# Optimization experiments

Hardware: AMD Instinct MI355X
Metric: run time of the kernel (lower is better)

## Reference

```python
import jax, jax.numpy as jnp
import numpy as np

N = 50000   # nodes
E = 600000  # edges (before self-loops)
D = 128     # input_dim
H = 128     # hidden_dim
NEG_SLOPE = 0.2  # GATConv default


def setup_inputs() -> dict:
    key = jax.random.key(0)
    ks = jax.random.split(key, 16)
    inp = {
        "x": jax.random.normal(ks[0], (N, D), jnp.float32),
        "edge_index": jax.random.randint(ks[1], (2, E), 0, N, dtype=jnp.int64),
        "edge_attr": jax.random.normal(ks[2], (E, 1), jnp.float32),
    }
    # GATConv params per layer: lin W [H,in] (no bias), att_src/att_dst [H],
    # lin_edge We [H,1] (no bias), att_edge [H], final bias b [H]
    def mk(k, shape, fan_in):
        return jax.random.normal(k, shape, jnp.float32) / np.sqrt(fan_in)
    ins = [D, H]
    ki = 3
    for i in range(2):
        cin = ins[i]
        inp[f"W{i}"] = mk(ks[ki], (H, cin), cin); ki += 1
        inp[f"att_src{i}"] = mk(ks[ki], (H,), H); ki += 1
        inp[f"att_dst{i}"] = mk(ks[ki], (H,), H); ki += 1
        inp[f"We{i}"] = mk(ks[ki], (H, 1), 1); ki += 1
        inp[f"att_e{i}"] = mk(ks[ki], (H,), H); ki += 1
        inp[f"b{i}"] = jnp.zeros((H,), jnp.float32)
    return inp


def _gat_forward(x, edge_index, edge_attr, params):
    # add self loops; self-loop edge_attr = mean of edge_attr (fill_value='mean')
    src = jnp.concatenate([edge_index[0], jnp.arange(N, dtype=edge_index.dtype)])
    dst = jnp.concatenate([edge_index[1], jnp.arange(N, dtype=edge_index.dtype)])
    ea = jnp.concatenate(
        [edge_attr, jnp.broadcast_to(edge_attr.mean(0, keepdims=True), (N, 1))], 0
    )  # [E+N, 1]

    def gat_layer(h, W, b, a_s, a_d, We, a_e):
        hp = h @ W.T                                   # [N, H]
        e_lin = ea @ We.T                              # [E+N, H]
        alpha = (hp @ a_s)[src] + (hp @ a_d)[dst] + e_lin @ a_e  # [E+N]
        alpha = jax.nn.leaky_relu(alpha, NEG_SLOPE)
        # segment softmax over destination nodes
        m = jax.ops.segment_max(alpha, dst, num_segments=N)
        m = jnp.where(jnp.isfinite(m), m, 0.0)
        w = jnp.exp(alpha - m[dst])
        denom = jax.ops.segment_sum(w, dst, num_segments=N)
        w = w / (denom[dst] + 1e-16)
        out = jax.ops.segment_sum(hp[src] * w[:, None], dst, num_segments=N)
        return out + b

    layer_outs = [x]
    h = x
    for i in range(2):
        h = jax.nn.relu(
            gat_layer(h, params[f"W{i}"], params[f"b{i}"], params[f"att_src{i}"],
                      params[f"att_dst{i}"], params[f"We{i}"], params[f"att_e{i}"])
        )
        layer_outs.append(h)
    return jnp.concatenate(layer_outs, axis=-1)  # JK 'cat': [N, D + 2H]


def reference(x, edge_index, edge_attr,
              W0, att_src0, att_dst0, We0, att_e0, b0,
              W1, att_src1, att_dst1, We1, att_e1, b1):
    params = {
        "W0": W0, "att_src0": att_src0, "att_dst0": att_dst0, "We0": We0,
        "att_e0": att_e0, "b0": b0,
        "W1": W1, "att_src1": att_src1, "att_dst1": att_dst1, "We1": We1,
        "att_e1": att_e1, "b1": b1,
    }
    return _gat_forward(x, edge_index, edge_attr, params)
```

## Files before the change

kernel.cpp:

```cpp
#include <hip/hip_runtime.h>
#include <hip/hip_fp16.h>
#include <math.h>

#define N_NODES 50000
#define N_EDGES 600000
#define TOT (N_EDGES + N_NODES)
#define HD 128
#define OUTW 384
#define NEG_SLOPE 0.2f

#define BM 128
#define GB 391
#define AGB 3125
#define NCHUNK 49
#define FILLB 256
#define XC 1563

#define DBLK 2540
#define WBLK 64
#define SBLK 64


typedef _Float16 h2_t __attribute__((ext_vector_type(2)));
typedef float f4_t __attribute__((ext_vector_type(4)));

static __device__ __forceinline__ float fdot2f(h2_t a, h2_t b, float c){
#if __has_builtin(__builtin_amdgcn_fdot2)
  return __builtin_amdgcn_fdot2(a, b, c, false);
#else
  return fmaf((float)a[0], (float)b[0], fmaf((float)a[1], (float)b[1], c));
#endif
}

static __device__ __forceinline__ void nt_store4(float* p, float a, float b, float c, float d){
  f4_t v = {a, b, c, d};
  __builtin_nontemporal_store(v, (f4_t*)p);
}

static __device__ __forceinline__ int load_edge(const void* ei, int is64, long long off){
  return is64 ? (int)((const long long*)ei)[off] : ((const int*)ei)[off];
}

__global__ __launch_bounds__(256) void edge_kernel(const void* ei, int* deg,
                                                   int* __restrict__ src32, int* __restrict__ dst32,
                                                   const float* __restrict__ W0, const float* __restrict__ W1,
                                                   __half2* __restrict__ Wt0, __half2* __restrict__ Wt1,
                                                   const float* __restrict__ eattr, float* scal,
                                                   const float* __restrict__ We0, const float* __restrict__ ae0,
                                                   const float* __restrict__ We1, const float* __restrict__ ae1){
  int b = blockIdx.x;
  int t = threadIdx.x;
  if (b < DBLK){
    __shared__ int s_is64;
    if (t < 64){
      long long v = ((const long long*)ei)[t];
      unsigned long long bad = __ballot(v < 0 || v >= N_NODES);
      if (t == 0) s_is64 = (bad == 0ull) ? 1 : 0;
    }
    __syncthreads();
    int is64 = s_is64;
    int e = b * 256 + t;
    if (e < TOT){
      int d;
      if (e < N_EDGES){
        int s = load_edge(ei, is64, e);
        d = load_edge(ei, is64, (long long)N_EDGES + e);
        src32[e] = s;
        dst32[e] = d;
      } else {
        d = e - N_EDGES;
      }
      atomicAdd(&deg[d], 1);
    }
  } else if (b < DBLK + WBLK){
    int e = (b - DBLK) * 256 + t;
    const float* W = (e < 8192) ? W0 : W1;
    __half2* Wt = (e < 8192) ? Wt0 : Wt1;
    int i = e & 8191;
    int n = i & 127, k2 = i >> 7;
    float a = W[n * HD + 2 * k2];
    float c = W[n * HD + 2 * k2 + 1];
    Wt[k2 * 128 + n] = __floats2half2_rn(a, c);
  } else if (b < DBLK + WBLK + SBLK){
    int gtid = (b - DBLK - WBLK) * 256 + t;
    float s = 0.f;
    for (int i = gtid; i < N_EDGES; i += SBLK * 256) s += eattr[i];
    #pragma unroll
    for (int o = 32; o > 0; o >>= 1) s += __shfl_down(s, o, 64);
    if ((t & 63) == 0) atomicAdd(&scal[0], s);
  } else {
    int w = t >> 6, lane = t & 63;
    if (w == 1){
      float s = We0[lane] * ae0[lane] + We0[lane + 64] * ae0[lane + 64];
      #pragma unroll
      for (int o = 32; o > 0; o >>= 1) s += __shfl_down(s, o, 64);
      if (lane == 0) scal[1] = s;
    } else if (w == 2){
      float s = We1[lane] * ae1[lane] + We1[lane + 64] * ae1[lane + 64];
      #pragma unroll
      for (int o = 32; o > 0; o >>= 1) s += __shfl_down(s, o, 64);
      if (lane == 0) scal[2] = s;
    }
  }
}

__global__ __launch_bounds__(256) void scanfuse_kernel(const int* __restrict__ deg,
                                                       int* __restrict__ rowstart,
                                                       int* __restrict__ rowcur,
                                                       int* chunkflag){
  __shared__ int sums[256];
  __shared__ int soff;
  int bid = blockIdx.x, t = threadIdx.x;
  int base = bid * 1024 + t * 4;
  int v[4];
  #pragma unroll
  for (int i = 0; i < 4; i++) v[i] = (base + i < N_NODES) ? deg[base + i] : 0;
  int tsum = v[0] + v[1] + v[2] + v[3];
  sums[t] = tsum;
  __syncthreads();
  for (int off = 1; off < 256; off <<= 1){
    int add = (t >= off) ? sums[t - off] : 0;
    __syncthreads();
    sums[t] += add;
    __syncthreads();
  }
  int run = sums[t] - tsum;

  if (t == 255)
    __hip_atomic_store(&chunkflag[bid], sums[255] + 1, __ATOMIC_RELEASE, __HIP_MEMORY_SCOPE_AGENT);

  if (t < 64){
    int acc_ = 0;
    for (int j = t; j < bid; j += 64){
      int val;
      long long spins = 0;
      while ((val = __hip_atomic_load(&chunkflag[j], __ATOMIC_ACQUIRE, __HIP_MEMORY_SCOPE_AGENT)) == 0){
        __builtin_amdgcn_s_sleep(1);
        if (++spins > (1LL << 24)) break;
      }
      acc_ += val - 1;
    }
    #pragma unroll
    for (int o = 32; o > 0; o >>= 1) acc_ += __shfl_down(acc_, o, 64);
    if (t == 0) soff = acc_;
  }
  __syncthreads();
  int off = soff;
  #pragma unroll
  for (int i = 0; i < 4; i++){
    if (base + i < N_NODES){
      int r = run + off;
      rowstart[base + i] = r;
      rowcur[base + i] = r;
    }
    run += v[i];
  }
}

template<bool F32>
__device__ __forceinline__ void gemm_tile512(int tb, int t, __half2* As2, __half2* Wh2,
                                             const void* __restrict__ hin,
                                             const __half2* __restrict__ Wt,
                                             __half* __restrict__ hp_h,
                                             const float* __restrict__ as_,
                                             const float* __restrict__ ad_,
                                             float* __restrict__ ssrc,
                                             float* __restrict__ sdst){
  int tx = t & 15;
  int ty = t >> 4;
  int rb = tb * BM;

  {
    const float4* src = (const float4*)Wt;
    float4* dst = (float4*)Wh2;
    #pragma unroll
    for (int p = 0; p < 4; p++) dst[t + p * 512] = src[t + p * 512];
  }
  if (F32){
    const float* xin = (const float*)hin;
    #pragma unroll
    for (int p = 0; p < 8; p++){
      int idx = t + p * 512;
      int row = idx >> 5, c4 = idx & 31;
      int gr = rb + row; if (gr >= N_NODES) gr = N_NODES - 1;
      float4 v = *(const float4*)&xin[(size_t)gr * HD + c4 * 4];
      As2[(2 * c4 + 0) * 128 + row] = __floats2half2_rn(v.x, v.y);
      As2[(2 * c4 + 1) * 128 + row] = __floats2half2_rn(v.z, v.w);
    }
  } else {
    const __half* hin16 = (const __half*)hin;
    #pragma unroll
    for (int p = 0; p < 4; p++){
      int idx = t + p * 512;
      int row = idx >> 4, c8 = idx & 15;
      int gr = rb + row; if (gr >= N_NODES) gr = N_NODES - 1;
      float4 v = *(const float4*)&hin16[(size_t)gr * HD + c8 * 8];
      __half2* hv = (__half2*)&v;
      #pragma unroll
      for (int q = 0; q < 4; q++) As2[(4 * c8 + q) * 128 + row] = hv[q];
    }
  }
  __syncthreads();

  float acc[4][8];
  #pragma unroll
  for (int i = 0; i < 4; i++)
    #pragma unroll
    for (int j = 0; j < 8; j++) acc[i][j] = 0.f;

  #pragma unroll 4
  for (int k2 = 0; k2 < 64; k2++){
    float4 ar0 = *(const float4*)&As2[k2 * 128 + ty * 4];
    float4 wr0 = *(const float4*)&Wh2[k2 * 128 + tx * 4];
    float4 wr1 = *(const float4*)&Wh2[k2 * 128 + 64 + tx * 4];
    const h2_t* av = (const h2_t*)&ar0;
    const h2_t* wv0 = (const h2_t*)&wr0;
    const h2_t* wv1 = (const h2_t*)&wr1;
    #pragma unroll
    for (int i = 0; i < 4; i++){
      h2_t ai = av[i];
      #pragma unroll
      for (int j = 0; j < 4; j++){
        acc[i][j]     = fdot2f(ai, wv0[j], acc[i][j]);
        acc[i][j + 4] = fdot2f(ai, wv1[j], acc[i][j + 4]);
      }
    }
  }

  #pragma unroll
  for (int i = 0; i < 4; i++){
    int r = rb + ty * 4 + i;
    if (r < N_NODES){
      float2 s0, s1;
      ((__half2*)&s0)[0] = __floats2half2_rn(acc[i][0], acc[i][1]);
      ((__half2*)&s0)[1] = __floats2half2_rn(acc[i][2], acc[i][3]);
      ((__half2*)&s1)[0] = __floats2half2_rn(acc[i][4], acc[i][5]);
      ((__half2*)&s1)[1] = __floats2half2_rn(acc[i][6], acc[i][7]);
      *(float2*)&hp_h[(size_t)r * HD + tx * 4]      = s0;
      *(float2*)&hp_h[(size_t)r * HD + 64 + tx * 4] = s1;
    }
  }

  float as_v[8], ad_v[8];
  #pragma unroll
  for (int j = 0; j < 4; j++){
    as_v[j]     = as_[tx * 4 + j];      ad_v[j]     = ad_[tx * 4 + j];
    as_v[j + 4] = as_[64 + tx * 4 + j]; ad_v[j + 4] = ad_[64 + tx * 4 + j];
  }
  #pragma unroll
  for (int i = 0; i < 4; i++){
    float ps = 0.f, pd = 0.f;
    #pragma unroll
    for (int j = 0; j < 8; j++){
      ps = fmaf(acc[i][j], as_v[j], ps);
      pd = fmaf(acc[i][j], ad_v[j], pd);
    }
    #pragma unroll
    for (int off = 8; off > 0; off >>= 1){
      ps += __shfl_down(ps, off, 16);
      pd += __shfl_down(pd, off, 16);
    }
    int r = rb + ty * 4 + i;
    if (tx == 0 && r < N_NODES){ ssrc[r] = ps; sdst[r] = pd; }
  }
}

__global__ __launch_bounds__(512, 4) void fillgemm_kernel(const float* __restrict__ x,
                                                          const __half2* __restrict__ Wt,
                                                          __half* __restrict__ hp_h,
                                                          const float* __restrict__ as_,
                                                          const float* __restrict__ ad_,
                                                          float* __restrict__ ssrc,
                                                          float* __restrict__ sdst,
                                                          const int* __restrict__ src32,
                                                          const int* __restrict__ dst32,
                                                          int* rowcur, int2* __restrict__ csr){
  __shared__ __align__(16) __half2 As2[64 * 128];
  __shared__ __align__(16) __half2 Wh2[64 * 128];
  int b = blockIdx.x;
  if (b < GB){
    gemm_tile512<true>(b, threadIdx.x, As2, Wh2, x, Wt, hp_h, as_, ad_, ssrc, sdst);
  } else {
    int gtid = (b - GB) * 512 + threadIdx.x;
    for (int e = gtid; e < TOT; e += FILLB * 512){
      int s, d;
      if (e < N_EDGES){
        s = src32[e];
        d = dst32[e];
      } else {
        s = d = e - N_EDGES;
      }
      int pos = atomicAdd(&rowcur[d], 1);
      csr[pos] = make_int2(s, e);
    }
  }
}

__global__ __launch_bounds__(512, 4) void gemm_kernel(const __half* __restrict__ hin,
                                                      const __half2* __restrict__ Wt,
                                                      __half* __restrict__ hp_h,
                                                      const float* __restrict__ as_,
                                                      const float* __restrict__ ad_,
                                                      float* __restrict__ ssrc,
                                                      float* __restrict__ sdst){
  __shared__ __align__(16) __half2 As2[64 * 128];
  __shared__ __align__(16) __half2 Wh2[64 * 128];
  gemm_tile512<false>(blockIdx.x, threadIdx.x, As2, Wh2, hin, Wt, hp_h, as_, ad_, ssrc, sdst);
}

__global__ __launch_bounds__(256) void agg_kernel(const int* __restrict__ rowstart,
                                                  const int2* __restrict__ csr,
                                                  const float* __restrict__ eattr,
                                                  const float* __restrict__ ssrc,
                                                  const float* __restrict__ sdst,
                                                  const float* __restrict__ scal, int which,
                                                  const __half* __restrict__ hp_h,
                                                  const float* __restrict__ bias,
                                                  __half* __restrict__ hnext,
                                                  float* __restrict__ out, int outoff,
                                                  const float* __restrict__ xsrc){
  int b = blockIdx.x;
  if (b >= AGB){
    int base = (b - AGB) * 1024 + threadIdx.x;
    #pragma unroll
    for (int u = 0; u < 4; u++){
      int idx = base + u * 256;
      if (idx < N_NODES * HD / 4){
        int n = idx >> 5, c4 = idx & 31;
        f4_t v = __builtin_nontemporal_load((const f4_t*)xsrc + idx);
        __builtin_nontemporal_store(v, (f4_t*)&out[(size_t)n * OUTW + c4 * 4]);
      }
    }
    return;
  }
  int sub  = threadIdx.x >> 4;
  int lane = threadIdx.x & 15;
  int n = b * 16 + sub;
  int s0 = rowstart[n];
  int s1 = (n + 1 < N_NODES) ? rowstart[n + 1] : TOT;
  float sd = sdst[n];
  float ce = scal[1 + which];
  float mean_ea = scal[0] * (1.0f / (float)N_EDGES);
  float4 bA = *(const float4*)&bias[lane * 8];
  float4 bB = *(const float4*)&bias[lane * 8 + 4];
  const float4* hb = (const float4*)hp_h;

  float a0 = 0.f, a1 = 0.f, a2 = 0.f, a3 = 0.f;
  float a4 = 0.f, a5 = 0.f, a6 = 0.f, a7 = 0.f;
  float sum = 0.f;

#define EW(se) ({ float eav = ((se).y < N_EDGES) ? eattr[(se).y] : mean_ea;       \
    float al = ssrc[(se).x] + sd + eav * ce;                                      \
    al = (al >= 0.f) ? al : NEG_SLOPE * al;                                       \
    expf(al); })

#define ACC8(r, p) { const __half2* hh = (const __half2*)&(r); float2 f;         \
    f = __half22float2(hh[0]); a0 = fmaf(p, f.x, a0); a1 = fmaf(p, f.y, a1);     \
    f = __half22float2(hh[1]); a2 = fmaf(p, f.x, a2); a3 = fmaf(p, f.y, a3);     \
    f = __half22float2(hh[2]); a4 = fmaf(p, f.x, a4); a5 = fmaf(p, f.y, a5);     \
    f = __half22float2(hh[3]); a6 = fmaf(p, f.x, a6); a7 = fmaf(p, f.y, a7); }

  int i = s0;
  for (; i + 8 <= s1; i += 8){
    int2 se[8]; float4 r[8];
    #pragma unroll
    for (int u = 0; u < 8; u++) se[u] = csr[i + u];
    #pragma unroll
    for (int u = 0; u < 8; u++) r[u] = hb[(size_t)se[u].x * 16 + lane];
    #pragma unroll
    for (int u = 0; u < 8; u++){
      float p = EW(se[u]);
      sum += p;
      ACC8(r[u], p);
    }
  }
  for (; i < s1; i++){
    int2 se = csr[i];
    float4 r = hb[(size_t)se.x * 16 + lane];
    float p = EW(se);
    sum += p;
    ACC8(r, p);
  }
#undef ACC8
#undef EW

  float inv = 1.0f / (sum + 1e-16f);
  float v0 = fmaf(a0, inv, bA.x); v0 = v0 > 0.f ? v0 : 0.f;
  float v1 = fmaf(a1, inv, bA.y); v1 = v1 > 0.f ? v1 : 0.f;
  float v2 = fmaf(a2, inv, bA.z); v2 = v2 > 0.f ? v2 : 0.f;
  float v3 = fmaf(a3, inv, bA.w); v3 = v3 > 0.f ? v3 : 0.f;
  float v4 = fmaf(a4, inv, bB.x); v4 = v4 > 0.f ? v4 : 0.f;
  float v5 = fmaf(a5, inv, bB.y); v5 = v5 > 0.f ? v5 : 0.f;
  float v6 = fmaf(a6, inv, bB.z); v6 = v6 > 0.f ? v6 : 0.f;
  float v7 = fmaf(a7, inv, bB.w); v7 = v7 > 0.f ? v7 : 0.f;
  if (hnext){
    float4 pk;
    __half2* p2h = (__half2*)&pk;
    p2h[0] = __floats2half2_rn(v0, v1);
    p2h[1] = __floats2half2_rn(v2, v3);
    p2h[2] = __floats2half2_rn(v4, v5);
    p2h[3] = __floats2half2_rn(v6, v7);
    *(float4*)&hnext[(size_t)n * HD + lane * 8] = pk;
  }
  nt_store4(&out[(size_t)n * OUTW + outoff + lane * 8],     v0, v1, v2, v3);
  nt_store4(&out[(size_t)n * OUTW + outoff + lane * 8 + 4], v4, v5, v6, v7);
}


extern "C" void kernel_launch(void* const* d_in, const int* in_sizes, int n_in,
                              void* d_out, int out_size, void* d_ws, size_t ws_size,
                              hipStream_t stream){
  (void)in_sizes; (void)n_in; (void)out_size; (void)ws_size;
  const float* x    = (const float*)d_in[0];
  const void*  ei   = d_in[1];
  const float* eatt = (const float*)d_in[2];
  const float* W0   = (const float*)d_in[3];
  const float* as0  = (const float*)d_in[4];
  const float* ad0  = (const float*)d_in[5];
  const float* We0  = (const float*)d_in[6];
  const float* ae0  = (const float*)d_in[7];
  const float* b0   = (const float*)d_in[8];
  const float* W1   = (const float*)d_in[9];
  const float* as1  = (const float*)d_in[10];
  const float* ad1  = (const float*)d_in[11];
  const float* We1  = (const float*)d_in[12];
  const float* ae1  = (const float*)d_in[13];
  const float* b1   = (const float*)d_in[14];
  float* out = (float*)d_out;

  char* ws = (char*)d_ws;
  size_t off = 0;
  auto alloc = [&](size_t bytes) -> void* {
    void* p = ws + off;
    off += (bytes + 255) & ~(size_t)255;
    return p;
  };
  __half*   hp_h     = (__half*)  alloc((size_t)N_NODES * HD * 2);
  __half*   h1       = (__half*)  alloc((size_t)N_NODES * HD * 2);
  float*    ssrc     = (float*)   alloc((size_t)N_NODES * 4);
  float*    sdst     = (float*)   alloc((size_t)N_NODES * 4);
  int*      deg      = (int*)     alloc((size_t)N_NODES * 4);
  float*    scal     = (float*)   alloc(256);
  int*      chunkflag= (int*)     alloc(256);
  int*      rowstart = (int*)     alloc((size_t)N_NODES * 4);
  int*      rowcur   = (int*)     alloc((size_t)N_NODES * 4);
  int*      src32    = (int*)     alloc((size_t)N_EDGES * 4);
  int*      dst32    = (int*)     alloc((size_t)N_EDGES * 4);
  int2*     csr      = (int2*)    alloc((size_t)TOT * 8);
  __half2*  Wt0      = (__half2*) alloc((size_t)8192 * 4);
  __half2*  Wt1      = (__half2*) alloc((size_t)8192 * 4);

  (void)hipMemsetAsync(deg, 0, 200192 + 256 + 256, stream);

  edge_kernel<<<DBLK + WBLK + SBLK + 1, 256, 0, stream>>>(
      ei, deg, src32, dst32, W0, W1, Wt0, Wt1, eatt, scal, We0, ae0, We1, ae1);
  scanfuse_kernel<<<NCHUNK, 256, 0, stream>>>(deg, rowstart, rowcur, chunkflag);

  fillgemm_kernel<<<GB + FILLB, 512, 0, stream>>>(x, Wt0, hp_h, as0, ad0, ssrc, sdst,
                                                  src32, dst32, rowcur, csr);
  agg_kernel<<<AGB + XC, 256, 0, stream>>>(rowstart, csr, eatt, ssrc, sdst, scal, 0,
                                           hp_h, b0, h1, out, 128, x);

  gemm_kernel<<<GB, 512, 0, stream>>>(h1, Wt1, hp_h, as1, ad1, ssrc, sdst);
  agg_kernel<<<AGB, 256, 0, stream>>>(rowstart, csr, eatt, ssrc, sdst, scal, 1,
                                      hp_h, b1, nullptr, out, 256, nullptr);
}
```

Measured before the change: 311.8 us.

## Split aggregation feature dimension into four column slices across blocks

```diff
diff --git a/kernel.cpp b/kernel.cpp
--- a/kernel.cpp
+++ b/kernel.cpp
@@ -11,10 +11,13 @@
 
 #define BM 128
 #define GB 391
-#define AGB 3125
 #define NCHUNK 49
 #define FILLB 256
 #define XC 1563
+
+#define NSL 4
+#define NG 1563
+#define AGB2 (NG * NSL)
 
 #define DBLK 2540
 #define WBLK 64
@@ -320,8 +323,8 @@
                                                   float* __restrict__ out, int outoff,
                                                   const float* __restrict__ xsrc){
   int b = blockIdx.x;
-  if (b >= AGB){
-    int base = (b - AGB) * 1024 + threadIdx.x;
+  if (b >= AGB2){
+    int base = (b - AGB2) * 1024 + threadIdx.x;
     #pragma unroll
     for (int u = 0; u < 4; u++){
       int idx = base + u * 256;
@@ -333,20 +336,23 @@
     }
     return;
   }
-  int sub  = threadIdx.x >> 4;
-  int lane = threadIdx.x & 15;
-  int n = b * 16 + sub;
+  int s   = b & 3;
+  int g   = b >> 2;
+  int sub = threadIdx.x >> 3;
+  int lane= threadIdx.x & 7;
+  int n = g * 32 + sub;
+  if (n >= N_NODES) return;
   int s0 = rowstart[n];
   int s1 = (n + 1 < N_NODES) ? rowstart[n + 1] : TOT;
   float sd = sdst[n];
   float ce = scal[1 + which];
   float mean_ea = scal[0] * (1.0f / (float)N_EDGES);
-  float4 bA = *(const float4*)&bias[lane * 8];
-  float4 bB = *(const float4*)&bias[lane * 8 + 4];
-  const float4* hb = (const float4*)hp_h;
+  int cb = s * 32 + lane * 4;
+  float4 b4 = *(const float4*)&bias[cb];
+  const float2* hb = (const float2*)hp_h;
+  size_t coff = (size_t)(cb >> 2);
 
   float a0 = 0.f, a1 = 0.f, a2 = 0.f, a3 = 0.f;
-  float a4 = 0.f, a5 = 0.f, a6 = 0.f, a7 = 0.f;
   float sum = 0.f;
 
 #define EW(se) ({ float eav = ((se).y < N_EDGES) ? eattr[(se).y] : mean_ea;       \
@@ -354,56 +360,47 @@
     al = (al >= 0.f) ? al : NEG_SLOPE * al;                                       \
     expf(al); })
 
-#define ACC8(r, p) { const __half2* hh = (const __half2*)&(r); float2 f;         \
+#define ACC4(r, p) { const __half2* hh = (const __half2*)&(r); float2 f;         \
     f = __half22float2(hh[0]); a0 = fmaf(p, f.x, a0); a1 = fmaf(p, f.y, a1);     \
-    f = __half22float2(hh[1]); a2 = fmaf(p, f.x, a2); a3 = fmaf(p, f.y, a3);     \
-    f = __half22float2(hh[2]); a4 = fmaf(p, f.x, a4); a5 = fmaf(p, f.y, a5);     \
-    f = __half22float2(hh[3]); a6 = fmaf(p, f.x, a6); a7 = fmaf(p, f.y, a7); }
+    f = __half22float2(hh[1]); a2 = fmaf(p, f.x, a2); a3 = fmaf(p, f.y, a3); }
 
   int i = s0;
   for (; i + 8 <= s1; i += 8){
-    int2 se[8]; float4 r[8];
+    int2 se[8]; float2 r[8];
     #pragma unroll
     for (int u = 0; u < 8; u++) se[u] = csr[i + u];
     #pragma unroll
-    for (int u = 0; u < 8; u++) r[u] = hb[(size_t)se[u].x * 16 + lane];
+    for (int u = 0; u < 8; u++) r[u] = hb[(size_t)se[u].x * 32 + coff];
     #pragma unroll
     for (int u = 0; u < 8; u++){
       float p = EW(se[u]);
       sum += p;
-      ACC8(r[u], p);
+      ACC4(r[u], p);
     }
   }
   for (; i < s1; i++){
     int2 se = csr[i];
-    float4 r = hb[(size_t)se.x * 16 + lane];
+    float2 r = hb[(size_t)se.x * 32 + coff];
     float p = EW(se);
     sum += p;
-    ACC8(r, p);
-  }
-#undef ACC8
+    ACC4(r, p);
+  }
+#undef ACC4
 #undef EW
 
   float inv = 1.0f / (sum + 1e-16f);
-  float v0 = fmaf(a0, inv, bA.x); v0 = v0 > 0.f ? v0 : 0.f;
-  float v1 = fmaf(a1, inv, bA.y); v1 = v1 > 0.f ? v1 : 0.f;
-  float v2 = fmaf(a2, inv, bA.z); v2 = v2 > 0.f ? v2 : 0.f;
-  float v3 = fmaf(a3, inv, bA.w); v3 = v3 > 0.f ? v3 : 0.f;
-  float v4 = fmaf(a4, inv, bB.x); v4 = v4 > 0.f ? v4 : 0.f;
-  float v5 = fmaf(a5, inv, bB.y); v5 = v5 > 0.f ? v5 : 0.f;
-  float v6 = fmaf(a6, inv, bB.z); v6 = v6 > 0.f ? v6 : 0.f;
-  float v7 = fmaf(a7, inv, bB.w); v7 = v7 > 0.f ? v7 : 0.f;
+  float v0 = fmaf(a0, inv, b4.x); v0 = v0 > 0.f ? v0 : 0.f;
+  float v1 = fmaf(a1, inv, b4.y); v1 = v1 > 0.f ? v1 : 0.f;
+  float v2 = fmaf(a2, inv, b4.z); v2 = v2 > 0.f ? v2 : 0.f;
+  float v3 = fmaf(a3, inv, b4.w); v3 = v3 > 0.f ? v3 : 0.f;
   if (hnext){
-    float4 pk;
+    float2 pk;
     __half2* p2h = (__half2*)&pk;
     p2h[0] = __floats2half2_rn(v0, v1);
     p2h[1] = __floats2half2_rn(v2, v3);
-    p2h[2] = __floats2half2_rn(v4, v5);
-    p2h[3] = __floats2half2_rn(v6, v7);
-    *(float4*)&hnext[(size_t)n * HD + lane * 8] = pk;
-  }
-  nt_store4(&out[(size_t)n * OUTW + outoff + lane * 8],     v0, v1, v2, v3);
-  nt_store4(&out[(size_t)n * OUTW + outoff + lane * 8 + 4], v4, v5, v6, v7);
+    *(float2*)&hnext[(size_t)n * HD + cb] = pk;
+  }
+  nt_store4(&out[(size_t)n * OUTW + outoff + cb], v0, v1, v2, v3);
 }
 
 
@@ -458,10 +455,10 @@
 
   fillgemm_kernel<<<GB + FILLB, 512, 0, stream>>>(x, Wt0, hp_h, as0, ad0, ssrc, sdst,
                                                   src32, dst32, rowcur, csr);
-  agg_kernel<<<AGB + XC, 256, 0, stream>>>(rowstart, csr, eatt, ssrc, sdst, scal, 0,
-                                           hp_h, b0, h1, out, 128, x);
+  agg_kernel<<<AGB2 + XC, 256, 0, stream>>>(rowstart, csr, eatt, ssrc, sdst, scal, 0,
+                                            hp_h, b0, h1, out, 128, x);
 
   gemm_kernel<<<GB, 512, 0, stream>>>(h1, Wt1, hp_h, as1, ad1, ssrc, sdst);
-  agg_kernel<<<AGB, 256, 0, stream>>>(rowstart, csr, eatt, ssrc, sdst, scal, 1,
-                                      hp_h, b1, nullptr, out, 256, nullptr);
-}
+  agg_kernel<<<AGB2, 256, 0, stream>>>(rowstart, csr, eatt, ssrc, sdst, scal, 1,
+                                       hp_h, b1, nullptr, out, 256, nullptr);
+}
```

Result: slower. 366.2 us (+17.5%).
